# Optimization experiments

Measured on AMD Instinct MI355X. Metric: run time of the kernel, lower is better.

Reference implementation:

```python
import jax, jax.numpy as jnp
import numpy as np

N_NODES = 50000
N_EDGES = 1600000
N_GRAPHS = 128
EDGE_DIM = 43
IN_DIM = 35
H = 128          # hidden_dim_1 = hidden_dim_2 = hidden_dim_3
G1, G2 = 64, 32  # gate MLP dims
H6, H7, H8 = 256, 128, 64
U0, U1 = 64, 64  # u_shape


def _linear_params(key, out_dim, in_dim):
    k1, k2 = jax.random.split(key)
    bound = 1.0 / np.sqrt(in_dim)
    W = jax.random.uniform(k1, (out_dim, in_dim), minval=-bound, maxval=bound, dtype=jnp.float32)
    b = jax.random.uniform(k2, (out_dim,), minval=-bound, maxval=bound, dtype=jnp.float32)
    return W, b


def setup_inputs() -> dict:
    key = jax.random.key(0)
    ks = jax.random.split(key, 24)
    x = jax.random.normal(ks[0], (N_NODES, IN_DIM), dtype=jnp.float32)
    edge_index = jax.random.randint(ks[1], (2, N_EDGES), 0, N_NODES, dtype=jnp.int64)
    edge_attr = jax.random.normal(ks[2], (N_EDGES, EDGE_DIM), dtype=jnp.float32)
    batch = jnp.sort(jax.random.randint(ks[3], (N_NODES,), 0, N_GRAPHS, dtype=jnp.int64))
    batch = batch.at[0].set(0).at[-1].set(N_GRAPHS - 1)
    u_soap = jax.random.normal(ks[4], (N_GRAPHS, U0), dtype=jnp.float32)
    u_dimer = jax.random.normal(ks[5], (N_GRAPHS, U1), dtype=jnp.float32)

    W1n, b1n = _linear_params(ks[6], H, IN_DIM + EDGE_DIM)
    W1r, b1r = _linear_params(ks[7], H, IN_DIM)
    W2n, b2n = _linear_params(ks[8], H, H + EDGE_DIM)
    W2r, b2r = _linear_params(ks[9], H, H)
    W3n, b3n = _linear_params(ks[10], H, H + EDGE_DIM)
    W3r, b3r = _linear_params(ks[11], H, H)
    Wg1, bg1 = _linear_params(ks[12], G1, H)
    Wg2, bg2 = _linear_params(ks[13], G2, G1)
    Wg3, bg3 = _linear_params(ks[14], 1, G2)
    Wl1, bl1 = _linear_params(ks[15], H6, U0 + U1 + H)
    Wl2, bl2 = _linear_params(ks[16], H7, H6)
    Wl3, bl3 = _linear_params(ks[17], H8, H7)
    Wl, bl = _linear_params(ks[18], 4, H8)

    return dict(x=x, edge_attr=edge_attr, u_soap=u_soap, u_dimer=u_dimer,
                W1n=W1n, b1n=b1n, W1r=W1r, b1r=b1r,
                W2n=W2n, b2n=b2n, W2r=W2r, b2r=b2r,
                W3n=W3n, b3n=b3n, W3r=W3r, b3r=b3r,
                Wg1=Wg1, bg1=bg1, Wg2=Wg2, bg2=bg2, Wg3=Wg3, bg3=bg3,
                Wl1=Wl1, bl1=bl1, Wl2=Wl2, bl2=bl2, Wl3=Wl3, bl3=bl3,
                Wl=Wl, bl=bl,
                edge_index=edge_index, batch=batch)


def _conv(x, src, edge_attr, Wn, bn, Wr, br):
    # gather source nodes, concat edge features, linear + tanh, scatter-add back to SOURCE (as in original)
    x_adj = jnp.tanh(jnp.concatenate([x[src], edge_attr], axis=1) @ Wn.T + bn)  # [E, H]
    neg_sum = jax.ops.segment_sum(x_adj, src, num_segments=N_NODES)             # [N, H]
    return jnp.tanh(x @ Wr.T + br) + neg_sum


def _segment_softmax(gate, batch, num_segments):
    m = jax.ops.segment_max(gate[:, 0], batch, num_segments=num_segments)
    g = jnp.exp(gate[:, 0] - m[batch])
    s = jax.ops.segment_sum(g, batch, num_segments=num_segments)
    return (g / (s[batch] + 1e-16))[:, None]


def reference(x, edge_attr, u_soap, u_dimer,
              W1n, b1n, W1r, b1r, W2n, b2n, W2r, b2r, W3n, b3n, W3r, b3r,
              Wg1, bg1, Wg2, bg2, Wg3, bg3,
              Wl1, bl1, Wl2, bl2, Wl3, bl3, Wl, bl,
              edge_index, batch):
    src = edge_index[0]
    h = _conv(x, src, edge_attr, W1n, b1n, W1r, b1r)
    h = _conv(h, src, edge_attr, W2n, b2n, W2r, b2r)
    h = _conv(h, src, edge_attr, W3n, b3n, W3r, b3r)

    # GlobalAttention readout
    g = jax.nn.relu(h @ Wg1.T + bg1)
    g = jax.nn.relu(g @ Wg2.T + bg2)
    gate = g @ Wg3.T + bg3                             # [N, 1]
    att = _segment_softmax(gate, batch, N_GRAPHS)      # [N, 1]
    embedding = jax.ops.segment_sum(att * h, batch, num_segments=N_GRAPHS)  # [G, H]

    u = jnp.concatenate([u_soap[:, :U0], u_dimer[:, :U1]], axis=1)
    e2 = jnp.concatenate([embedding, u], axis=1)
    out = jax.nn.relu(e2 @ Wl1.T + bl1)
    out = jax.nn.relu(out @ Wl2.T + bl2)
    out = jax.nn.relu(out @ Wl3.T + bl3)
    out4 = out @ Wl.T + bl                             # [G, 4]
    pred_last = out4.sum(axis=1, keepdims=True)
    return jnp.concatenate([out4, pred_last], axis=1), att
```

## Files before the change

### kernel.cpp

```cpp
#include <hip/hip_runtime.h>
#include <cstdint>
#include <cstddef>

#define N_NODES_C 50000
#define N_EDGES_C 1600000
#define N_GRAPHS_C 128
#define EDGE_DIM_C 43
#define IN_DIM_C 35
#define HDIM_C 128
#define MAXG_C 150000

typedef _Float16 f16x8 __attribute__((ext_vector_type(8)));
typedef float f32x4 __attribute__((ext_vector_type(4)));

__device__ __forceinline__ float fast_tanh(float x) {
    float xc = fminf(9.0f, fmaxf(-9.0f, x));
    float t = __expf(2.0f * xc);
    return (t - 1.0f) * __builtin_amdgcn_rcpf(t + 1.0f);
}

#define TANH_K 2.8853900817779268f

__device__ __forceinline__ float exp2f_fast(float x) {
#if __has_builtin(__builtin_amdgcn_exp2f)
    return __builtin_amdgcn_exp2f(x);
#else
    return __expf(x * 0.69314718055994531f);
#endif
}

__device__ __forceinline__ float tanh_from_arg(float a) {
    float t = exp2f_fast(a);
    return fmaf(-2.0f, __builtin_amdgcn_rcpf(t + 1.0f), 1.0f);
}


__global__ __launch_bounds__(256) void hist_kernel(const int* __restrict__ src,
                                                   int* __restrict__ cnt) {
    int i = blockIdx.x * 256 + threadIdx.x;
    if (i < N_EDGES_C) atomicAdd(&cnt[src[i]], 1);
}

__global__ __launch_bounds__(1024) void scan_kernel(const int* __restrict__ cnt,
                                                    int* __restrict__ rowptr,
                                                    int* __restrict__ work,
                                                    int* __restrict__ growptr,
                                                    int* __restrict__ ngroups) {
    __shared__ int wsumA[16], wsumB[16];
    __shared__ int carryA, carryB;
    int t = threadIdx.x;
    int lane = t & 63, wid = t >> 6;
    if (t == 0) { carryA = 0; carryB = 0; }
    __syncthreads();
    for (int base = 0; base < N_NODES_C; base += 4096) {
        int i0 = base + t * 4;
        int v[4], u[4];
        #pragma unroll
        for (int j = 0; j < 4; ++j) {
            int i = i0 + j;
            v[j] = (i < N_NODES_C) ? cnt[i] : 0;
            u[j] = (v[j] + 15) >> 4;
        }
        int pv[4], pu[4];
        pv[0] = 0; pu[0] = 0;
        #pragma unroll
        for (int j = 1; j < 4; ++j) { pv[j] = pv[j-1] + v[j-1]; pu[j] = pu[j-1] + u[j-1]; }
        int tA = pv[3] + v[3], tB = pu[3] + u[3];
        int x = tA, y = tB;
        #pragma unroll
        for (int off = 1; off < 64; off <<= 1) {
            int xx = __shfl_up(x, off, 64);
            int yy = __shfl_up(y, off, 64);
            if (lane >= off) { x += xx; y += yy; }
        }
        if (lane == 63) { wsumA[wid] = x; wsumB[wid] = y; }
        __syncthreads();
        if (wid == 0) {
            int wa = (lane < 16) ? wsumA[lane] : 0;
            int wb = (lane < 16) ? wsumB[lane] : 0;
            #pragma unroll
            for (int off = 1; off < 16; off <<= 1) {
                int aa = __shfl_up(wa, off, 64);
                int bb = __shfl_up(wb, off, 64);
                if (lane >= off) { wa += aa; wb += bb; }
            }
            if (lane < 16) { wsumA[lane] = wa; wsumB[lane] = wb; }
        }
        __syncthreads();
        int exA = carryA + (wid ? wsumA[wid - 1] : 0) + x - tA;
        int exB = carryB + (wid ? wsumB[wid - 1] : 0) + y - tB;
        #pragma unroll
        for (int j = 0; j < 4; ++j) {
            int i = i0 + j;
            if (i < N_NODES_C) {
                int rv = exA + pv[j];
                rowptr[i] = rv; work[i] = rv;
                growptr[i] = exB + pu[j];
            }
        }
        int totA = wsumA[15], totB = wsumB[15];
        __syncthreads();
        if (t == 0) { carryA += totA; carryB += totB; }
        __syncthreads();
    }
    if (t == 0) {
        rowptr[N_NODES_C] = carryA;
        growptr[N_NODES_C] = carryB;
        ngroups[0] = carryB;
    }
}

__global__ __launch_bounds__(256) void scatter_kernel(const int* __restrict__ src,
                                                      int* __restrict__ work,
                                                      int* __restrict__ eord) {
    int i = blockIdx.x * 256 + threadIdx.x;
    if (i < N_EDGES_C) {
        int s = src[i];
        int pos = atomicAdd(&work[s], 1);
        eord[pos] = i;
    }
}

__global__ __launch_bounds__(256) void graph_misc(const int* __restrict__ rowptr,
                                                  const int* __restrict__ growptr,
                                                  const int* __restrict__ batch,
                                                  int2* __restrict__ gdesc,
                                                  int* __restrict__ grp) {
    int i = blockIdx.x * 256 + threadIdx.x;
    if (i < N_NODES_C) {
        int rp = rowptr[i];
        int deg = rowptr[i + 1] - rp;
        int gp = growptr[i];
        int ngr = (deg + 15) >> 4;
        for (int gi = 0; gi < ngr; ++gi) {
            int valid = deg - gi * 16; if (valid > 16) valid = 16;
            gdesc[gp + gi] = make_int2(i | (valid << 16), rp + gi * 16);
        }
    }
    if (i <= N_GRAPHS_C) {
        int lo = 0, hi = N_NODES_C;
        while (lo < hi) {
            int mid = (lo + hi) >> 1;
            if (batch[mid] < i) lo = mid + 1; else hi = mid;
        }
        grp[i] = lo;
    }
}

__global__ __launch_bounds__(256) void ea2h(const float* __restrict__ EA,
                                            _Float16* __restrict__ EAh) {
    int t = threadIdx.x;
    int e = blockIdx.x * 64 + (t >> 2);
    int q = t & 3;
    if (e >= N_EDGES_C) return;
    const float* pe = EA + (size_t)e * EDGE_DIM_C;
    unsigned int pk[6];
    #pragma unroll
    for (int jj = 0; jj < 6; ++jj) {
        int c0 = q * 12 + 2 * jj;
        float v0 = (c0 < EDGE_DIM_C) ? pe[c0] : 0.0f;
        float v1 = (c0 + 1 < EDGE_DIM_C) ? pe[c0 + 1] : 0.0f;
        unsigned short h0 = __builtin_bit_cast(unsigned short, (_Float16)v0);
        unsigned short h1 = __builtin_bit_cast(unsigned short, (_Float16)v1);
        pk[jj] = (unsigned int)h0 | ((unsigned int)h1 << 16);
    }
    unsigned int* outp = (unsigned int*)(EAh + (size_t)e * 48 + q * 12);
    *(uint2*)(outp)     = make_uint2(pk[0], pk[1]);
    *(uint2*)(outp + 2) = make_uint2(pk[2], pk[3]);
    *(uint2*)(outp + 4) = make_uint2(pk[4], pk[5]);
}


#define BKN 32
__global__ __launch_bounds__(256) void node_gemm(
    const float* __restrict__ A, int K,
    const float* __restrict__ Wn, int ldn, const float* __restrict__ bn,
    const float* __restrict__ Wr, const float* __restrict__ br,
    float* __restrict__ Base, float* __restrict__ Root)
{
    __shared__ float At[BKN][64];
    __shared__ float Bw[BKN][128];
    int t = threadIdx.x;
    int z = blockIdx.y;
    const float* W = z ? Wr : Wn;
    int ldW = z ? K : ldn;
    const float* bias = z ? br : bn;
    float* Out = z ? Root : Base;

    int m0 = blockIdx.x * 64;
    int tn4 = (t % 32) * 4;
    int tm8 = (t / 32) * 8;
    float acc[8][4];
    #pragma unroll
    for (int a = 0; a < 8; a++)
        #pragma unroll
        for (int b = 0; b < 4; b++) acc[a][b] = 0.0f;

    int nkc = (K + BKN - 1) / BKN;
    for (int c = 0; c < nkc; c++) {
        int kc = c * BKN;
        {
            int m_l = t >> 2;
            int q = t & 3;
            int m = m0 + m_l;
            #pragma unroll
            for (int ii = 0; ii < 8; ii++) {
                int kk = q * 8 + ii;
                int k = kc + kk;
                float v = 0.0f;
                if (m < N_NODES_C && k < K) v = A[(size_t)m * K + k];
                At[kk][m_l] = v;
            }
        }
        {
            int j = t % 128;
            int kg2 = t / 128;
            #pragma unroll
            for (int ii = 0; ii < 16; ii++) {
                int kk = kg2 * 16 + ii;
                int k = kc + kk;
                float v = 0.0f;
                if (k < K) v = W[(size_t)j * ldW + k];
                Bw[kk][j] = v;
            }
        }
        __syncthreads();
        #pragma unroll
        for (int kk = 0; kk < BKN; kk++) {
            float a[8], b[4];
            #pragma unroll
            for (int mi = 0; mi < 8; mi++) a[mi] = At[kk][tm8 + mi];
            #pragma unroll
            for (int ni = 0; ni < 4; ni++) b[ni] = Bw[kk][tn4 + ni];
            #pragma unroll
            for (int mi = 0; mi < 8; mi++)
                #pragma unroll
                for (int ni = 0; ni < 4; ni++)
                    acc[mi][ni] = fmaf(a[mi], b[ni], acc[mi][ni]);
        }
        __syncthreads();
    }

    float4 bv = *(const float4*)&bias[tn4];
    #pragma unroll
    for (int mi = 0; mi < 8; mi++) {
        int m = m0 + tm8 + mi;
        if (m < N_NODES_C) {
            float4 o;
            o.x = acc[mi][0] + bv.x;
            o.y = acc[mi][1] + bv.y;
            o.z = acc[mi][2] + bv.z;
            o.w = acc[mi][3] + bv.w;
            if (z) { o.x = fast_tanh(o.x); o.y = fast_tanh(o.y); o.z = fast_tanh(o.z); o.w = fast_tanh(o.w); }
            *(float4*)&Out[(size_t)m * HDIM_C + tn4] = o;
        }
    }
}


__global__ __launch_bounds__(256) void edge_mfma(
    const _Float16* __restrict__ EAh, const int* __restrict__ eord,
    const int2* __restrict__ gdesc, const int* __restrict__ ngroups,
    const float* __restrict__ Base,
    const float* __restrict__ Wfull, int colOff, int ldW,
    float* __restrict__ Hout)
{
    int t = threadIdx.x;
    int lane = t & 63, wid = t >> 6;
    int l15 = lane & 15, quad = lane >> 4;

    f16x8 bf[8][2];
    #pragma unroll
    for (int nt = 0; nt < 8; ++nt) {
        const float* wr = Wfull + (size_t)(nt * 16 + l15) * ldW + colOff;
        #pragma unroll
        for (int kt = 0; kt < 2; ++kt) {
            f16x8 b;
            #pragma unroll
            for (int j = 0; j < 8; ++j) {
                int k = kt * 32 + quad * 8 + j;
                float v = (k < EDGE_DIM_C) ? wr[k] : 0.0f;
                b[j] = (_Float16)v;
            }
            bf[nt][kt] = b;
        }
    }

    bool useA1 = (quad < 2);
    int off0 = quad * 8;
    int off1 = 32 + ((quad & 1) * 8);
    int rbase = quad * 4;

    int NG = ngroups[0];
    int W = gridDim.x * 4;
    int g = blockIdx.x * 4 + wid;
    if (g >= NG) return;

    f16x8 zz8 = {};
    int2 d0 = gdesc[g];
    int2 d1 = (g + W < NG) ? gdesc[g + W] : make_int2(0, 0);
    int2 d2 = (g + 2 * W < NG) ? gdesc[g + 2 * W] : make_int2(0, 0);
    int e0 = (l15 < (d0.x >> 16)) ? eord[d0.y + l15] : -1;
    int e1 = (l15 < (d1.x >> 16)) ? eord[d1.y + l15] : -1;
    f16x8 a0 = zz8, a1 = zz8;
    if (e0 >= 0) {
        const _Float16* ap = EAh + (size_t)e0 * 48;
        a0 = *(const f16x8*)(ap + off0);
        if (useA1) a1 = *(const f16x8*)(ap + off1);
    }

    while (true) {
        int n = d0.x & 0xFFFF;
        int valid = d0.x >> 16;

        int gn3 = g + 3 * W;
        int2 d3 = (gn3 < NG) ? gdesc[gn3] : make_int2(0, 0);
        int e2 = (l15 < (d2.x >> 16)) ? eord[d2.y + l15] : -1;
        f16x8 p0 = zz8, p1 = zz8;
        if (e1 >= 0) {
            const _Float16* ap = EAh + (size_t)e1 * 48;
            p0 = *(const f16x8*)(ap + off0);
            if (useA1) p1 = *(const f16x8*)(ap + off1);
        }
        const float* bp = Base + (size_t)n * HDIM_C;
        float b2[8];
        #pragma unroll
        for (int nt = 0; nt < 8; ++nt) b2[nt] = TANH_K * bp[nt * 16 + l15];

        f32x4 acc[8];
        #pragma unroll
        for (int nt = 0; nt < 8; ++nt) {
            f32x4 zz = {0.f, 0.f, 0.f, 0.f};
            acc[nt] = __builtin_amdgcn_mfma_f32_16x16x32_f16(a0, bf[nt][0], zz, 0, 0, 0);
            acc[nt] = __builtin_amdgcn_mfma_f32_16x16x32_f16(a1, bf[nt][1], acc[nt], 0, 0, 0);
        }
        float cs[8];
        if (valid == 16) {
            #pragma unroll
            for (int nt = 0; nt < 8; ++nt) {
                float s = tanh_from_arg(fmaf(TANH_K, acc[nt][0], b2[nt]));
                s += tanh_from_arg(fmaf(TANH_K, acc[nt][1], b2[nt]));
                s += tanh_from_arg(fmaf(TANH_K, acc[nt][2], b2[nt]));
                s += tanh_from_arg(fmaf(TANH_K, acc[nt][3], b2[nt]));
                cs[nt] = s;
            }
        } else {
            int rq = valid - rbase;
            #pragma unroll
            for (int nt = 0; nt < 8; ++nt) {
                float s = 0.0f;
                #pragma unroll
                for (int r = 0; r < 4; ++r) {
                    float v = tanh_from_arg(fmaf(TANH_K, acc[nt][r], b2[nt]));
                    s += (r < rq) ? v : 0.0f;
                }
                cs[nt] = s;
            }
        }

        #pragma unroll
        for (int nt = 0; nt < 8; ++nt) {
            cs[nt] += __shfl_xor(cs[nt], 16, 64);
            cs[nt] += __shfl_xor(cs[nt], 32, 64);
        }
        float v0, v1;
        if (quad == 0)      { v0 = cs[0]; v1 = cs[1]; }
        else if (quad == 1) { v0 = cs[2]; v1 = cs[3]; }
        else if (quad == 2) { v0 = cs[4]; v1 = cs[5]; }
        else                { v0 = cs[6]; v1 = cs[7]; }
        int c0 = quad * 32 + l15;
        float* hp = Hout + (size_t)n * HDIM_C;
        unsafeAtomicAdd(hp + c0, v0);
        unsafeAtomicAdd(hp + c0 + 16, v1);

        g += W;
        if (g >= NG) break;
        d0 = d1; d1 = d2; d2 = d3;
        a0 = p0; a1 = p1;
        e1 = e2;
    }
}


__global__ __launch_bounds__(256) void gate_kernel(
    const float* __restrict__ h,
    const float* __restrict__ Wg1, const float* __restrict__ bg1,
    const float* __restrict__ Wg2, const float* __restrict__ bg2,
    const float* __restrict__ Wg3, const float* __restrict__ bg3,
    float* __restrict__ gate)
{
    __shared__ float Ht[128][65];
    __shared__ float G1[64][65];
    __shared__ float G2[32][65];
    int t = threadIdx.x;
    int m0 = blockIdx.x * 64;
    #pragma unroll
    for (int ii = 0; ii < 32; ++ii) {
        int flat = ii * 256 + t;
        int k = flat & 127, m = flat >> 7;
        float v = (m0 + m < N_NODES_C) ? h[(size_t)(m0 + m) * HDIM_C + k] : 0.0f;
        Ht[k][m] = v;
    }
    __syncthreads();
    int m = t & 63, slab = t >> 6;
    {
        float a[16];
        #pragma unroll
        for (int jj = 0; jj < 16; ++jj) a[jj] = bg1[slab * 16 + jj];
        for (int k = 0; k < 128; ++k) {
            float hv = Ht[k][m];
            #pragma unroll
            for (int jj = 0; jj < 16; ++jj)
                a[jj] = fmaf(Wg1[(size_t)(slab * 16 + jj) * 128 + k], hv, a[jj]);
        }
        #pragma unroll
        for (int jj = 0; jj < 16; ++jj) G1[slab * 16 + jj][m] = fmaxf(a[jj], 0.0f);
    }
    __syncthreads();
    {
        float b[8];
        #pragma unroll
        for (int jj = 0; jj < 8; ++jj) b[jj] = bg2[slab * 8 + jj];
        for (int k = 0; k < 64; ++k) {
            float gv = G1[k][m];
            #pragma unroll
            for (int jj = 0; jj < 8; ++jj)
                b[jj] = fmaf(Wg2[(size_t)(slab * 8 + jj) * 64 + k], gv, b[jj]);
        }
        #pragma unroll
        for (int jj = 0; jj < 8; ++jj) G2[slab * 8 + jj][m] = fmaxf(b[jj], 0.0f);
    }
    __syncthreads();
    if (t < 64 && m0 + t < N_NODES_C) {
        float s = bg3[0];
        #pragma unroll
        for (int k = 0; k < 32; ++k) s = fmaf(Wg3[k], G2[k][t], s);
        gate[m0 + t] = s;
    }
}


__global__ __launch_bounds__(256) void graph_attn(
    const float* __restrict__ gate, const int* __restrict__ grp,
    const float* __restrict__ h3, float* __restrict__ att_out,
    float* __restrict__ emb)
{
    int g = blockIdx.x;
    int t = threadIdx.x;
    int s = grp[g], e = grp[g + 1];
    __shared__ float red[256];
    __shared__ float attb[256];

    float m = -3.4e38f;
    for (int i = s + t; i < e; i += 256) m = fmaxf(m, gate[i]);
    red[t] = m;
    __syncthreads();
    #pragma unroll
    for (int off = 128; off >= 1; off >>= 1) {
        if (t < off) red[t] = fmaxf(red[t], red[t + off]);
        __syncthreads();
    }
    m = red[0];
    __syncthreads();

    float sum = 0.0f;
    for (int i = s + t; i < e; i += 256) sum += __expf(gate[i] - m);
    red[t] = sum;
    __syncthreads();
    #pragma unroll
    for (int off = 128; off >= 1; off >>= 1) {
        if (t < off) red[t] += red[t + off];
        __syncthreads();
    }
    float scale = 1.0f / (red[0] + 1e-16f);
    __syncthreads();

    int j = t & 127;
    int half = t >> 7;
    float acc = 0.0f;
    for (int base = s; base < e; base += 256) {
        int i = base + t;
        float a = 0.0f;
        if (i < e) {
            a = __expf(gate[i] - m) * scale;
            att_out[i] = a;
        }
        attb[t] = a;
        __syncthreads();
        int cnt = e - base; if (cnt > 256) cnt = 256;
        for (int r = half; r < cnt; r += 2)
            acc = fmaf(attb[r], h3[(size_t)(base + r) * HDIM_C + j], acc);
        __syncthreads();
    }
    red[t] = acc;
    __syncthreads();
    if (t < 128) emb[(size_t)g * 128 + t] = red[t] + red[t + 128];
}


__global__ __launch_bounds__(256) void final_mlp(
    const float* __restrict__ emb, const float* __restrict__ us, const float* __restrict__ ud,
    const float* __restrict__ Wl1, const float* __restrict__ bl1,
    const float* __restrict__ Wl2, const float* __restrict__ bl2,
    const float* __restrict__ Wl3, const float* __restrict__ bl3,
    const float* __restrict__ Wl, const float* __restrict__ bl,
    float* __restrict__ out5)
{
    int g = blockIdx.x;
    int t = threadIdx.x;
    __shared__ float e2[256], o1[256], o2[128], o3[64], o4[4];
    if (t < 128) e2[t] = emb[(size_t)g * 128 + t];
    else if (t < 192) e2[t] = us[(size_t)g * 64 + (t - 128)];
    else e2[t] = ud[(size_t)g * 64 + (t - 192)];
    __syncthreads();
    {
        float s = bl1[t];
        const float* wr = Wl1 + (size_t)t * 256;
        #pragma unroll 8
        for (int k = 0; k < 256; k++) s = fmaf(wr[k], e2[k], s);
        o1[t] = fmaxf(s, 0.0f);
    }
    __syncthreads();
    if (t < 128) {
        float s = bl2[t];
        const float* wr = Wl2 + (size_t)t * 256;
        #pragma unroll 8
        for (int k = 0; k < 256; k++) s = fmaf(wr[k], o1[k], s);
        o2[t] = fmaxf(s, 0.0f);
    }
    __syncthreads();
    if (t < 64) {
        float s = bl3[t];
        const float* wr = Wl3 + (size_t)t * 128;
        #pragma unroll 8
        for (int k = 0; k < 128; k++) s = fmaf(wr[k], o2[k], s);
        o3[t] = fmaxf(s, 0.0f);
    }
    __syncthreads();
    if (t < 4) {
        float s = bl[t];
        const float* wr = Wl + (size_t)t * 64;
        #pragma unroll 8
        for (int k = 0; k < 64; k++) s = fmaf(wr[k], o3[k], s);
        o4[t] = s;
    }
    __syncthreads();
    if (t < 5) {
        float v = (t < 4) ? o4[t] : (o4[0] + o4[1] + o4[2] + o4[3]);
        out5[(size_t)g * 5 + t] = v;
    }
}


extern "C" void kernel_launch(void* const* d_in, const int* in_sizes, int n_in,
                              void* d_out, int out_size, void* d_ws, size_t ws_size,
                              hipStream_t stream) {
    const float* x       = (const float*)d_in[0];
    const float* ea      = (const float*)d_in[1];
    const float* u_soap  = (const float*)d_in[2];
    const float* u_dimer = (const float*)d_in[3];
    const float* W1n = (const float*)d_in[4];   const float* b1n = (const float*)d_in[5];
    const float* W1r = (const float*)d_in[6];   const float* b1r = (const float*)d_in[7];
    const float* W2n = (const float*)d_in[8];   const float* b2n = (const float*)d_in[9];
    const float* W2r = (const float*)d_in[10];  const float* b2r = (const float*)d_in[11];
    const float* W3n = (const float*)d_in[12];  const float* b3n = (const float*)d_in[13];
    const float* W3r = (const float*)d_in[14];  const float* b3r = (const float*)d_in[15];
    const float* Wg1 = (const float*)d_in[16];  const float* bg1 = (const float*)d_in[17];
    const float* Wg2 = (const float*)d_in[18];  const float* bg2 = (const float*)d_in[19];
    const float* Wg3 = (const float*)d_in[20];  const float* bg3 = (const float*)d_in[21];
    const float* Wl1 = (const float*)d_in[22];  const float* bl1 = (const float*)d_in[23];
    const float* Wl2 = (const float*)d_in[24];  const float* bl2 = (const float*)d_in[25];
    const float* Wl3 = (const float*)d_in[26];  const float* bl3 = (const float*)d_in[27];
    const float* Wl  = (const float*)d_in[28];  const float* bl  = (const float*)d_in[29];
    const int* eidx  = (const int*)d_in[30];
    const int* batch = (const int*)d_in[31];
    const int* src = eidx;

    float* out5 = (float*)d_out;
    float* att  = out5 + (size_t)N_GRAPHS_C * 5;

    char* p = (char*)d_ws;
    size_t off = 0;
    auto alloc = [&](size_t bytes) -> void* {
        void* r = p + off;
        off += (bytes + 255) & ~(size_t)255;
        return r;
    };
    int* cnt     = (int*)alloc((size_t)N_NODES_C * 4);
    int* rowptr  = (int*)alloc((size_t)(N_NODES_C + 1) * 4);
    int* growptr = (int*)alloc((size_t)(N_NODES_C + 1) * 4);
    int* work    = (int*)alloc((size_t)N_NODES_C * 4);
    int* eord    = (int*)alloc((size_t)(N_EDGES_C + 64) * 4);
    int* grp     = (int*)alloc((size_t)(N_GRAPHS_C + 1) * 4);
    int* ngroups = (int*)alloc(256);
    int2* gdesc  = (int2*)alloc((size_t)MAXG_C * 8);
    float* gate  = (float*)alloc((size_t)N_NODES_C * 4);
    float* emb   = (float*)alloc((size_t)N_GRAPHS_C * 128 * 4);
    float* bufA  = (float*)alloc((size_t)N_NODES_C * HDIM_C * 4);
    float* bufB  = (float*)alloc((size_t)N_NODES_C * HDIM_C * 4);
    float* bufC  = (float*)alloc((size_t)N_NODES_C * HDIM_C * 4);
    _Float16* EAh = (_Float16*)alloc((size_t)N_EDGES_C * 48 * 2);

    hipMemsetAsync(cnt, 0, (size_t)N_NODES_C * 4, stream);

    int eblocks = (N_EDGES_C + 255) / 256;
    ea2h<<<(N_EDGES_C + 63) / 64, 256, 0, stream>>>(ea, EAh);
    hist_kernel<<<eblocks, 256, 0, stream>>>(src, cnt);
    scan_kernel<<<1, 1024, 0, stream>>>(cnt, rowptr, work, growptr, ngroups);
    scatter_kernel<<<eblocks, 256, 0, stream>>>(src, work, eord);
    graph_misc<<<(N_NODES_C + 255) / 256, 256, 0, stream>>>(rowptr, growptr, batch, gdesc, grp);

    dim3 ng((N_NODES_C + 63) / 64, 2);
    int egrid = 1024;

    node_gemm<<<ng, 256, 0, stream>>>(x, IN_DIM_C, W1n, IN_DIM_C + EDGE_DIM_C, b1n, W1r, b1r, bufA, bufB);
    edge_mfma<<<egrid, 256, 0, stream>>>(EAh, eord, gdesc, ngroups, bufA, W1n, IN_DIM_C, IN_DIM_C + EDGE_DIM_C, bufB);
    node_gemm<<<ng, 256, 0, stream>>>(bufB, HDIM_C, W2n, HDIM_C + EDGE_DIM_C, b2n, W2r, b2r, bufA, bufC);
    edge_mfma<<<egrid, 256, 0, stream>>>(EAh, eord, gdesc, ngroups, bufA, W2n, HDIM_C, HDIM_C + EDGE_DIM_C, bufC);
    node_gemm<<<ng, 256, 0, stream>>>(bufC, HDIM_C, W3n, HDIM_C + EDGE_DIM_C, b3n, W3r, b3r, bufA, bufB);
    edge_mfma<<<egrid, 256, 0, stream>>>(EAh, eord, gdesc, ngroups, bufA, W3n, HDIM_C, HDIM_C + EDGE_DIM_C, bufB);

    gate_kernel<<<(N_NODES_C + 63) / 64, 256, 0, stream>>>(bufB, Wg1, bg1, Wg2, bg2, Wg3, bg3, gate);
    graph_attn<<<N_GRAPHS_C, 256, 0, stream>>>(gate, grp, bufB, att, emb);
    final_mlp<<<N_GRAPHS_C, 256, 0, stream>>>(emb, u_soap, u_dimer,
                                              Wl1, bl1, Wl2, bl2, Wl3, bl3, Wl, bl, out5);
}
```

Before: 1.573 ms.

## Pre-permute edge attributes into group-slot order so edge kernels read contiguously

The scatter pass now records each edge's padded slot (group*16 + row) instead of an edge-order index. A permute kernel then writes the fp16 edge attributes straight into a group-blocked buffer. Each edge_mfma layer can therefore load its 16-edge tiles contiguously, with no eord indirection and with a smaller 4-byte group descriptor. Work is also assigned in contiguous group ranges per wave rather than grid-strided, which improves locality for the destination-row atomics. Padding slots in the permuted buffer are never zeroed, so partial groups read uninitialised fp16 data, and correctness depends on the partial-group path masking those lanes.

New measurement: 1.581 ms. About the same (+0.5%).

```diff
diff --git a/kernel.cpp b/kernel.cpp
--- a/kernel.cpp
+++ b/kernel.cpp
@@ -112,19 +112,22 @@
 
 __global__ __launch_bounds__(256) void scatter_kernel(const int* __restrict__ src,
                                                       int* __restrict__ work,
-                                                      int* __restrict__ eord) {
+                                                      const int* __restrict__ rowptr,
+                                                      const int* __restrict__ growptr,
+                                                      int* __restrict__ pslot) {
     int i = blockIdx.x * 256 + threadIdx.x;
     if (i < N_EDGES_C) {
         int s = src[i];
         int pos = atomicAdd(&work[s], 1);
-        eord[pos] = i;
+        int r = pos - rowptr[s];
+        pslot[i] = (growptr[s] << 4) + r;
     }
 }
 
 __global__ __launch_bounds__(256) void graph_misc(const int* __restrict__ rowptr,
                                                   const int* __restrict__ growptr,
                                                   const int* __restrict__ batch,
-                                                  int2* __restrict__ gdesc,
+                                                  int* __restrict__ gdesc,
                                                   int* __restrict__ grp) {
     int i = blockIdx.x * 256 + threadIdx.x;
     if (i < N_NODES_C) {
@@ -134,7 +137,7 @@
         int ngr = (deg + 15) >> 4;
         for (int gi = 0; gi < ngr; ++gi) {
             int valid = deg - gi * 16; if (valid > 16) valid = 16;
-            gdesc[gp + gi] = make_int2(i | (valid << 16), rp + gi * 16);
+            gdesc[gp + gi] = i | (valid << 16);
         }
     }
     if (i <= N_GRAPHS_C) {
@@ -147,12 +150,14 @@
     }
 }
 
-__global__ __launch_bounds__(256) void ea2h(const float* __restrict__ EA,
-                                            _Float16* __restrict__ EAh) {
+__global__ __launch_bounds__(256) void permute_ea(const float* __restrict__ EA,
+                                                  const int* __restrict__ pslot,
+                                                  _Float16* __restrict__ EAp) {
     int t = threadIdx.x;
     int e = blockIdx.x * 64 + (t >> 2);
     int q = t & 3;
     if (e >= N_EDGES_C) return;
+    int slot = pslot[e];
     const float* pe = EA + (size_t)e * EDGE_DIM_C;
     unsigned int pk[6];
     #pragma unroll
@@ -164,7 +169,7 @@
         unsigned short h1 = __builtin_bit_cast(unsigned short, (_Float16)v1);
         pk[jj] = (unsigned int)h0 | ((unsigned int)h1 << 16);
     }
-    unsigned int* outp = (unsigned int*)(EAh + (size_t)e * 48 + q * 12);
+    unsigned int* outp = (unsigned int*)(EAp + (size_t)slot * 48 + q * 12);
     *(uint2*)(outp)     = make_uint2(pk[0], pk[1]);
     *(uint2*)(outp + 2) = make_uint2(pk[2], pk[3]);
     *(uint2*)(outp + 4) = make_uint2(pk[4], pk[5]);
@@ -259,8 +264,8 @@
 
 
 __global__ __launch_bounds__(256) void edge_mfma(
-    const _Float16* __restrict__ EAh, const int* __restrict__ eord,
-    const int2* __restrict__ gdesc, const int* __restrict__ ngroups,
+    const _Float16* __restrict__ EAp, const int* __restrict__ gdesc,
+    const int* __restrict__ ngroups,
     const float* __restrict__ Base,
     const float* __restrict__ Wfull, int colOff, int ldW,
     float* __restrict__ Hout)
@@ -290,38 +295,35 @@
     int off0 = quad * 8;
     int off1 = 32 + ((quad & 1) * 8);
     int rbase = quad * 4;
+    int aoff = l15 * 48;
 
     int NG = ngroups[0];
-    int W = gridDim.x * 4;
-    int g = blockIdx.x * 4 + wid;
+    int TOT = gridDim.x * 4;
+    int per = (NG + TOT - 1) / TOT;
+    int g = (blockIdx.x * 4 + wid) * per;
     if (g >= NG) return;
+    int gend = g + per; if (gend > NG) gend = NG;
 
     f16x8 zz8 = {};
-    int2 d0 = gdesc[g];
-    int2 d1 = (g + W < NG) ? gdesc[g + W] : make_int2(0, 0);
-    int2 d2 = (g + 2 * W < NG) ? gdesc[g + 2 * W] : make_int2(0, 0);
-    int e0 = (l15 < (d0.x >> 16)) ? eord[d0.y + l15] : -1;
-    int e1 = (l15 < (d1.x >> 16)) ? eord[d1.y + l15] : -1;
-    f16x8 a0 = zz8, a1 = zz8;
-    if (e0 >= 0) {
-        const _Float16* ap = EAh + (size_t)e0 * 48;
-        a0 = *(const f16x8*)(ap + off0);
-        if (useA1) a1 = *(const f16x8*)(ap + off1);
-    }
-
-    while (true) {
-        int n = d0.x & 0xFFFF;
-        int valid = d0.x >> 16;
-
-        int gn3 = g + 3 * W;
-        int2 d3 = (gn3 < NG) ? gdesc[gn3] : make_int2(0, 0);
-        int e2 = (l15 < (d2.x >> 16)) ? eord[d2.y + l15] : -1;
+    int d0 = gdesc[g];
+    const _Float16* ap = EAp + (size_t)g * 768 + aoff;
+    f16x8 a0 = *(const f16x8*)(ap + off0);
+    f16x8 a1 = useA1 ? *(const f16x8*)(ap + off1) : zz8;
+
+    for (;;) {
+        int g1 = g + 1;
+        int d1 = 0;
         f16x8 p0 = zz8, p1 = zz8;
-        if (e1 >= 0) {
-            const _Float16* ap = EAh + (size_t)e1 * 48;
-            p0 = *(const f16x8*)(ap + off0);
-            if (useA1) p1 = *(const f16x8*)(ap + off1);
-        }
+        if (g1 < gend) {
+            d1 = gdesc[g1];
+            const _Float16* apn = EAp + (size_t)g1 * 768 + aoff;
+            p0 = *(const f16x8*)(apn + off0);
+            if (useA1) p1 = *(const f16x8*)(apn + off1);
+        }
+
+        int n = d0 & 0xFFFF;
+        int valid = d0 >> 16;
+
         const float* bp = Base + (size_t)n * HDIM_C;
         float b2[8];
         #pragma unroll
@@ -373,11 +375,9 @@
         unsafeAtomicAdd(hp + c0, v0);
         unsafeAtomicAdd(hp + c0 + 16, v1);
 
-        g += W;
-        if (g >= NG) break;
-        d0 = d1; d1 = d2; d2 = d3;
+        if (g1 >= gend) break;
+        g = g1; d0 = d1;
         a0 = p0; a1 = p1;
-        e1 = e2;
     }
 }
 
@@ -590,35 +590,35 @@
     int* rowptr  = (int*)alloc((size_t)(N_NODES_C + 1) * 4);
     int* growptr = (int*)alloc((size_t)(N_NODES_C + 1) * 4);
     int* work    = (int*)alloc((size_t)N_NODES_C * 4);
-    int* eord    = (int*)alloc((size_t)(N_EDGES_C + 64) * 4);
+    int* pslot   = (int*)alloc((size_t)N_EDGES_C * 4);
     int* grp     = (int*)alloc((size_t)(N_GRAPHS_C + 1) * 4);
     int* ngroups = (int*)alloc(256);
-    int2* gdesc  = (int2*)alloc((size_t)MAXG_C * 8);
+    int* gdesc   = (int*)alloc((size_t)MAXG_C * 4);
     float* gate  = (float*)alloc((size_t)N_NODES_C * 4);
     float* emb   = (float*)alloc((size_t)N_GRAPHS_C * 128 * 4);
     float* bufA  = (float*)alloc((size_t)N_NODES_C * HDIM_C * 4);
     float* bufB  = (float*)alloc((size_t)N_NODES_C * HDIM_C * 4);
     float* bufC  = (float*)alloc((size_t)N_NODES_C * HDIM_C * 4);
-    _Float16* EAh = (_Float16*)alloc((size_t)N_EDGES_C * 48 * 2);
+    _Float16* EAp = (_Float16*)alloc((size_t)MAXG_C * 768 * 2);
 
     hipMemsetAsync(cnt, 0, (size_t)N_NODES_C * 4, stream);
 
     int eblocks = (N_EDGES_C + 255) / 256;
-    ea2h<<<(N_EDGES_C + 63) / 64, 256, 0, stream>>>(ea, EAh);
     hist_kernel<<<eblocks, 256, 0, stream>>>(src, cnt);
     scan_kernel<<<1, 1024, 0, stream>>>(cnt, rowptr, work, growptr, ngroups);
-    scatter_kernel<<<eblocks, 256, 0, stream>>>(src, work, eord);
+    scatter_kernel<<<eblocks, 256, 0, stream>>>(src, work, rowptr, growptr, pslot);
     graph_misc<<<(N_NODES_C + 255) / 256, 256, 0, stream>>>(rowptr, growptr, batch, gdesc, grp);
+    permute_ea<<<(N_EDGES_C + 63) / 64, 256, 0, stream>>>(ea, pslot, EAp);
 
     dim3 ng((N_NODES_C + 63) / 64, 2);
     int egrid = 1024;
 
     node_gemm<<<ng, 256, 0, stream>>>(x, IN_DIM_C, W1n, IN_DIM_C + EDGE_DIM_C, b1n, W1r, b1r, bufA, bufB);
-    edge_mfma<<<egrid, 256, 0, stream>>>(EAh, eord, gdesc, ngroups, bufA, W1n, IN_DIM_C, IN_DIM_C + EDGE_DIM_C, bufB);
+    edge_mfma<<<egrid, 256, 0, stream>>>(EAp, gdesc, ngroups, bufA, W1n, IN_DIM_C, IN_DIM_C + EDGE_DIM_C, bufB);
     node_gemm<<<ng, 256, 0, stream>>>(bufB, HDIM_C, W2n, HDIM_C + EDGE_DIM_C, b2n, W2r, b2r, bufA, bufC);
-    edge_mfma<<<egrid, 256, 0, stream>>>(EAh, eord, gdesc, ngroups, bufA, W2n, HDIM_C, HDIM_C + EDGE_DIM_C, bufC);
+    edge_mfma<<<egrid, 256, 0, stream>>>(EAp, gdesc, ngroups, bufA, W2n, HDIM_C, HDIM_C + EDGE_DIM_C, bufC);
     node_gemm<<<ng, 256, 0, stream>>>(bufC, HDIM_C, W3n, HDIM_C + EDGE_DIM_C, b3n, W3r, b3r, bufA, bufB);
-    edge_mfma<<<egrid, 256, 0, stream>>>(EAh, eord, gdesc, ngroups, bufA, W3n, HDIM_C, HDIM_C + EDGE_DIM_C, bufB);
+    edge_mfma<<<egrid, 256, 0, stream>>>(EAp, gdesc, ngroups, bufA, W3n, HDIM_C, HDIM_C + EDGE_DIM_C, bufB);
 
     gate_kernel<<<(N_NODES_C + 63) / 64, 256, 0, stream>>>(bufB, Wg1, bg1, Wg2, bg2, Wg3, bg3, gate);
     graph_attn<<<N_GRAPHS_C, 256, 0, stream>>>(gate, grp, bufB, att, emb);
```
